# Optimization experiments

Measured on AMD Instinct MI355X. Metric: run time of the kernel, lower is better.

The kernel has to match this reference:

```python
import jax, jax.numpy as jnp
import numpy as np

NS, NC = 4, 3
DIAG = 4.1  # 4 + mass (mass = 0.1)
LAT = (16, 16, 16, 16)  # T, Z, Y, X


def setup_inputs() -> dict:
    key = jax.random.key(0)
    ks = jax.random.split(key, 6)
    psi_shape = LAT + (NS, NC)
    K_shape = (4,) + LAT + (NS * NC, NS * NC)
    return {
        "psi_re": jax.random.normal(ks[0], psi_shape, dtype=jnp.float32),
        "psi_im": jax.random.normal(ks[1], psi_shape, dtype=jnp.float32),
        "K_fwd_re": jax.random.normal(ks[2], K_shape, dtype=jnp.float32),
        "K_fwd_im": jax.random.normal(ks[3], K_shape, dtype=jnp.float32),
        "K_bwd_re": jax.random.normal(ks[4], K_shape, dtype=jnp.float32),
        "K_bwd_im": jax.random.normal(ks[5], K_shape, dtype=jnp.float32),
    }


def reference(psi_re, psi_im, K_fwd_re, K_fwd_im, K_bwd_re, K_bwd_im):
    # Flatten spin-color: (T,Z,Y,X,ns,nc) -> (T,Z,Y,X,ns*nc)
    pr = psi_re.reshape(psi_re.shape[:-2] + (NS * NC,))
    pi = psi_im.reshape(psi_im.shape[:-2] + (NS * NC,))
    out_re = DIAG * pr
    out_im = DIAG * pi
    for mu in range(4):
        ldim = mu - 5  # T,Z,Y,X axes of pr (which has 5 dims)
        Kfr, Kfi = K_fwd_re[mu], K_fwd_im[mu]
        Kbr, Kbi = K_bwd_re[mu], K_bwd_im[mu]
        pf_re = jnp.roll(pr, -1, axis=ldim)
        pf_im = jnp.roll(pi, -1, axis=ldim)
        pb_re = jnp.roll(pr, 1, axis=ldim)
        pb_im = jnp.roll(pi, 1, axis=ldim)
        # Complex 12x12 matvec per site: (K_re + i K_im) @ (p_re + i p_im)
        cf_re = jnp.einsum('...ij,...j->...i', Kfr, pf_re) - jnp.einsum('...ij,...j->...i', Kfi, pf_im)
        cf_im = jnp.einsum('...ij,...j->...i', Kfr, pf_im) + jnp.einsum('...ij,...j->...i', Kfi, pf_re)
        cb_re = jnp.einsum('...ij,...j->...i', Kbr, pb_re) - jnp.einsum('...ij,...j->...i', Kbi, pb_im)
        cb_im = jnp.einsum('...ij,...j->...i', Kbr, pb_im) + jnp.einsum('...ij,...j->...i', Kbi, pb_re)
        out_re = out_re - 0.5 * (cf_re + cb_re)
        out_im = out_im - 0.5 * (cf_im + cb_im)
    out_re = out_re.reshape(out_re.shape[:-1] + (NS, NC))
    out_im = out_im.reshape(out_im.shape[:-1] + (NS, NC))
    return (out_re, out_im)
```

## Files before the change

kernel.cpp:

```cpp
#include <hip/hip_runtime.h>

#define VOL   65536
#define NSC   12
#define DIAG  4.1f
#define SPB   16
#define THREADS (SPB * NSC)
#define MATF  (SPB * 144)

#define CMADD(kr, ki, vr, vi)                                              \
    sr += kr.x * vr.x - ki.x * vi.x;  si += kr.x * vi.x + ki.x * vr.x;     \
    sr += kr.y * vr.y - ki.y * vi.y;  si += kr.y * vi.y + ki.y * vr.y;     \
    sr += kr.z * vr.z - ki.z * vi.z;  si += kr.z * vi.z + ki.z * vr.z;     \
    sr += kr.w * vr.w - ki.w * vi.w;  si += kr.w * vi.w + ki.w * vr.w;

__device__ __forceinline__ void g2lds16(const float* g, float* l) {
    __builtin_amdgcn_global_load_lds(
        (const __attribute__((address_space(1))) unsigned int*)g,
        (__attribute__((address_space(3))) unsigned int*)l,
        16, 0, 0);
}

__global__ __launch_bounds__(THREADS) void dslash_kernel(
    const float* __restrict__ psi_re, const float* __restrict__ psi_im,
    const float* __restrict__ Kf_re,  const float* __restrict__ Kf_im,
    const float* __restrict__ Kb_re,  const float* __restrict__ Kb_im,
    float* __restrict__ out_re,       float* __restrict__ out_im)
{
    __shared__ float lds[4 * MATF];

    const int j  = threadIdx.x;
    const int w  = j >> 6;
    const int l  = j & 63;
    const int site0 = blockIdx.x * SPB;
    const int sl = j / NSC;
    const int i  = j - sl * NSC;
    const int site = site0 + sl;

    const int x = site        & 15;
    const int y = (site >> 4) & 15;
    const int z = (site >> 8) & 15;
    const int t = (site >> 12) & 15;
    const int coords [4] = {t, z, y, x};
    const int strides[4] = {4096, 256, 16, 1};

    float acc_re = DIAG * psi_re[site * NSC + i];
    float acc_im = DIAG * psi_im[site * NSC + i];

    const float* __restrict__ Ks[4] = {Kf_re, Kf_im, Kb_re, Kb_im};

    for (int mu = 0; mu < 4; ++mu) {
        const size_t gbase = ((size_t)mu * VOL + (size_t)site0) * 144;
        #pragma unroll
        for (int m = 0; m < 4; ++m) {
            const float* src = Ks[m] + gbase;
            #pragma unroll
            for (int jj = 0; jj < 3; ++jj) {
                const int c = jj * 3 + w;
                g2lds16(src + c * 256 + l * 4, &lds[m * MATF + c * 256 + l * 4]);
            }
        }
        __syncthreads();

        const int cc = coords[mu], st = strides[mu];
        const int base = site - cc * st;
        const int sf = base + ((cc + 1)  & 15) * st;
        const int sb = base + ((cc + 15) & 15) * st;

        const float4* kfr = (const float4*)&lds[0 * MATF + j * 12];
        const float4* kfi = (const float4*)&lds[1 * MATF + j * 12];
        const float4* kbr = (const float4*)&lds[2 * MATF + j * 12];
        const float4* kbi = (const float4*)&lds[3 * MATF + j * 12];

        const float4* pfr = (const float4*)(psi_re + sf * NSC);
        const float4* pfi = (const float4*)(psi_im + sf * NSC);
        const float4* pbr = (const float4*)(psi_re + sb * NSC);
        const float4* pbi = (const float4*)(psi_im + sb * NSC);

        float sr = 0.f, si = 0.f;
        #pragma unroll
        for (int q = 0; q < 3; ++q) {
            const float4 a  = kfr[q], b  = kfi[q];
            const float4 vr = pfr[q], vi = pfi[q];
            CMADD(a, b, vr, vi);
            const float4 c4 = kbr[q], d4 = kbi[q];
            const float4 wr = pbr[q], wi = pbi[q];
            CMADD(c4, d4, wr, wi);
        }
        acc_re -= 0.5f * sr;
        acc_im -= 0.5f * si;
        __syncthreads();
    }

    out_re[site * NSC + i] = acc_re;
    out_im[site * NSC + i] = acc_im;
}

extern "C" void kernel_launch(void* const* d_in, const int* in_sizes, int n_in,
                              void* d_out, int out_size, void* d_ws, size_t ws_size,
                              hipStream_t stream) {
    const float* psi_re = (const float*)d_in[0];
    const float* psi_im = (const float*)d_in[1];
    const float* Kf_re  = (const float*)d_in[2];
    const float* Kf_im  = (const float*)d_in[3];
    const float* Kb_re  = (const float*)d_in[4];
    const float* Kb_im  = (const float*)d_in[5];

    float* out_re = (float*)d_out;
    float* out_im = (float*)d_out + (size_t)VOL * NSC;

    const int grid = VOL / SPB;

    dslash_kernel<<<grid, THREADS, 0, stream>>>(psi_re, psi_im,
                                                Kf_re, Kf_im, Kb_re, Kb_im,
                                                out_re, out_im);
}
```

Before: 114.7 us.

## Double-buffer link-matrix staging per direction and stage neighbor spinors in LDS

Splits the per-mu load of four 12x12 matrices into eight half-phases (forward and backward) and double-buffers them in LDS. The next phase's global-to-LDS copy is issued while the current phase computes, with explicit vmcnt waits and barriers. Each block is one x-line, so the seven needed psi lines (its own line plus the t, z and y neighbors) are loaded once into LDS, and x-neighbors come from a wraparound index. This removes the scattered global psi reads and the load-then-compute serialization, at the cost of more barriers and more LDS per block, which may lower occupancy.

```diff
diff --git a/kernel.cpp b/kernel.cpp
--- a/kernel.cpp
+++ b/kernel.cpp
@@ -4,8 +4,11 @@
 #define NSC   12
 #define DIAG  4.1f
 #define SPB   16
-#define THREADS (SPB * NSC)
+#define THREADS 192
 #define MATF  (SPB * 144)
+#define STGF  (2 * MATF)
+#define PSI_LINE 192
+#define PSI_F (7 * 2 * PSI_LINE)
 
 #define CMADD(kr, ki, vr, vi)                                              \
     sr += kr.x * vr.x - ki.x * vi.x;  si += kr.x * vi.x + ki.x * vr.x;     \
@@ -20,79 +23,122 @@
         16, 0, 0);
 }
 
+template<int P>
+__device__ __forceinline__ void stage(const float* Kf_re, const float* Kf_im,
+                                      const float* Kb_re, const float* Kb_im,
+                                      int site0, int w, int l, float* kb) {
+    constexpr int mu = P >> 1;
+    const float* re = (P & 1) ? Kb_re : Kf_re;
+    const float* im = (P & 1) ? Kb_im : Kf_im;
+    const size_t gb = ((size_t)mu * VOL + (size_t)site0) * 144;
+    #pragma unroll
+    for (int jj = 0; jj < 3; ++jj) {
+        const int c = jj * 3 + w;
+        g2lds16(re + gb + c * 256 + l * 4, kb + 0 * MATF + c * 256 + l * 4);
+        g2lds16(im + gb + c * 256 + l * 4, kb + 1 * MATF + c * 256 + l * 4);
+    }
+}
+
+template<int P>
+__device__ __forceinline__ void phase_compute(const float* kb, const float* pb,
+                                              int sl, int j,
+                                              float& acc_re, float& acc_im) {
+    constexpr int mu = P >> 1;
+    constexpr int d  = P & 1;
+    constexpr int line = (mu < 3) ? (1 + mu * 2 + d) : 0;
+    const int sidx = (mu < 3) ? sl : (d == 0 ? (sl + 1) & 15 : (sl + 15) & 15);
+
+    const float4* kr = (const float4*)(kb + j * 12);
+    const float4* ki = (const float4*)(kb + MATF + j * 12);
+    const float4* vr = (const float4*)(pb + (line * 2 + 0) * PSI_LINE + sidx * 12);
+    const float4* vi = (const float4*)(pb + (line * 2 + 1) * PSI_LINE + sidx * 12);
+
+    float sr = 0.f, si = 0.f;
+    #pragma unroll
+    for (int q = 0; q < 3; ++q) {
+        const float4 a = kr[q], b = ki[q];
+        const float4 x = vr[q], y4 = vi[q];
+        CMADD(a, b, x, y4);
+    }
+    acc_re -= 0.5f * sr;
+    acc_im -= 0.5f * si;
+}
+
+#define WAITV(n) asm volatile("s_waitcnt vmcnt(" #n ")" ::: "memory")
+#define CFENCE() asm volatile("" ::: "memory")
+
 __global__ __launch_bounds__(THREADS) void dslash_kernel(
     const float* __restrict__ psi_re, const float* __restrict__ psi_im,
     const float* __restrict__ Kf_re,  const float* __restrict__ Kf_im,
     const float* __restrict__ Kb_re,  const float* __restrict__ Kb_im,
     float* __restrict__ out_re,       float* __restrict__ out_im)
 {
-    __shared__ float lds[4 * MATF];
+    __shared__ float kbuf[2][STGF];
+    __shared__ float pbuf[PSI_F];
 
     const int j  = threadIdx.x;
     const int w  = j >> 6;
     const int l  = j & 63;
-    const int site0 = blockIdx.x * SPB;
     const int sl = j / NSC;
-    const int i  = j - sl * NSC;
-    const int site = site0 + sl;
+    const int lid = blockIdx.x;
+    const int site0 = lid * SPB;
 
-    const int x = site        & 15;
-    const int y = (site >> 4) & 15;
-    const int z = (site >> 8) & 15;
-    const int t = (site >> 12) & 15;
-    const int coords [4] = {t, z, y, x};
-    const int strides[4] = {4096, 256, 16, 1};
+    const int y = lid & 15, z = (lid >> 4) & 15, t = (lid >> 8) & 15;
 
-    float acc_re = DIAG * psi_re[site * NSC + i];
-    float acc_im = DIAG * psi_im[site * NSC + i];
+    int lb[7];
+    lb[0] = lid * 192;
+    lb[1] = ((((t + 1)  & 15) << 8) | (z << 4) | y) * 192;
+    lb[2] = ((((t + 15) & 15) << 8) | (z << 4) | y) * 192;
+    lb[3] = ((t << 8) | (((z + 1)  & 15) << 4) | y) * 192;
+    lb[4] = ((t << 8) | (((z + 15) & 15) << 4) | y) * 192;
+    lb[5] = ((t << 8) | (z << 4) | ((y + 1)  & 15)) * 192;
+    lb[6] = ((t << 8) | (z << 4) | ((y + 15) & 15)) * 192;
 
-    const float* __restrict__ Ks[4] = {Kf_re, Kf_im, Kb_re, Kb_im};
+    #pragma unroll
+    for (int r = 0; r < 4; ++r) {
+        const int idx = j + r * THREADS;
+        if (idx < 672) {
+            const int c  = idx % 48;
+            const int la = idx / 48;
+            const int ar = la & 1, ln = la >> 1;
+            const float4 v = *(const float4*)((ar ? psi_im : psi_re) + lb[ln] + c * 4);
+            *(float4*)&pbuf[(ln * 2 + ar) * PSI_LINE + c * 4] = v;
+        }
+    }
+    __syncthreads();
 
-    for (int mu = 0; mu < 4; ++mu) {
-        const size_t gbase = ((size_t)mu * VOL + (size_t)site0) * 144;
-        #pragma unroll
-        for (int m = 0; m < 4; ++m) {
-            const float* src = Ks[m] + gbase;
-            #pragma unroll
-            for (int jj = 0; jj < 3; ++jj) {
-                const int c = jj * 3 + w;
-                g2lds16(src + c * 256 + l * 4, &lds[m * MATF + c * 256 + l * 4]);
-            }
-        }
-        __syncthreads();
+    float acc_re = DIAG * pbuf[0 * PSI_LINE + j];
+    float acc_im = DIAG * pbuf[1 * PSI_LINE + j];
 
-        const int cc = coords[mu], st = strides[mu];
-        const int base = site - cc * st;
-        const int sf = base + ((cc + 1)  & 15) * st;
-        const int sb = base + ((cc + 15) & 15) * st;
+    stage<0>(Kf_re, Kf_im, Kb_re, Kb_im, site0, w, l, kbuf[0]);
+    stage<1>(Kf_re, Kf_im, Kb_re, Kb_im, site0, w, l, kbuf[1]);
 
-        const float4* kfr = (const float4*)&lds[0 * MATF + j * 12];
-        const float4* kfi = (const float4*)&lds[1 * MATF + j * 12];
-        const float4* kbr = (const float4*)&lds[2 * MATF + j * 12];
-        const float4* kbi = (const float4*)&lds[3 * MATF + j * 12];
+#define DO_PHASE(P, NWAIT)                                                    \
+    WAITV(NWAIT);                                                             \
+    __builtin_amdgcn_s_barrier();                                             \
+    CFENCE();                                                                 \
+    phase_compute<P>(kbuf[(P) & 1], pbuf, sl, j, acc_re, acc_im);             \
+    CFENCE();                                                                 \
+    __builtin_amdgcn_s_barrier();                                             \
+    CFENCE();
 
-        const float4* pfr = (const float4*)(psi_re + sf * NSC);
-        const float4* pfi = (const float4*)(psi_im + sf * NSC);
-        const float4* pbr = (const float4*)(psi_re + sb * NSC);
-        const float4* pbi = (const float4*)(psi_im + sb * NSC);
+    DO_PHASE(0, 6)
+    stage<2>(Kf_re, Kf_im, Kb_re, Kb_im, site0, w, l, kbuf[0]);
+    DO_PHASE(1, 6)
+    stage<3>(Kf_re, Kf_im, Kb_re, Kb_im, site0, w, l, kbuf[1]);
+    DO_PHASE(2, 6)
+    stage<4>(Kf_re, Kf_im, Kb_re, Kb_im, site0, w, l, kbuf[0]);
+    DO_PHASE(3, 6)
+    stage<5>(Kf_re, Kf_im, Kb_re, Kb_im, site0, w, l, kbuf[1]);
+    DO_PHASE(4, 6)
+    stage<6>(Kf_re, Kf_im, Kb_re, Kb_im, site0, w, l, kbuf[0]);
+    DO_PHASE(5, 6)
+    stage<7>(Kf_re, Kf_im, Kb_re, Kb_im, site0, w, l, kbuf[1]);
+    DO_PHASE(6, 6)
+    DO_PHASE(7, 0)
 
-        float sr = 0.f, si = 0.f;
-        #pragma unroll
-        for (int q = 0; q < 3; ++q) {
-            const float4 a  = kfr[q], b  = kfi[q];
-            const float4 vr = pfr[q], vi = pfi[q];
-            CMADD(a, b, vr, vi);
-            const float4 c4 = kbr[q], d4 = kbi[q];
-            const float4 wr = pbr[q], wi = pbi[q];
-            CMADD(c4, d4, wr, wi);
-        }
-        acc_re -= 0.5f * sr;
-        acc_im -= 0.5f * si;
-        __syncthreads();
-    }
-
-    out_re[site * NSC + i] = acc_re;
-    out_im[site * NSC + i] = acc_im;
+    out_re[site0 * NSC + j] = acc_re;
+    out_im[site0 * NSC + j] = acc_im;
 }
 
 extern "C" void kernel_launch(void* const* d_in, const int* in_sizes, int n_in,
@@ -108,9 +154,7 @@
     float* out_re = (float*)d_out;
     float* out_im = (float*)d_out + (size_t)VOL * NSC;
 
-    const int grid = VOL / SPB;
-
-    dslash_kernel<<<grid, THREADS, 0, stream>>>(psi_re, psi_im,
-                                                Kf_re, Kf_im, Kb_re, Kb_im,
-                                                out_re, out_im);
+    dslash_kernel<<<VOL / SPB, THREADS, 0, stream>>>(psi_re, psi_im,
+                                                     Kf_re, Kf_im, Kb_re, Kb_im,
+                                                     out_re, out_im);
 }
```

Result: no change. 113.7 us (-0.9%).
